# Performance work log

Measured on AMD Instinct MI355X. Metric: run time of the kernel, lower is better.

Reference implementation:

```python
import jax, jax.numpy as jnp
import numpy as np

B, F, D, M = 1024, 64, 256, 32
K = D // 3  # kWTA winners
LN_EPS = 1e-3  # keras LayerNormalization default


def setup_inputs() -> dict:
    key = jax.random.key(0)
    ks = jax.random.split(key, 8)
    in_dim = F * 2 * D  # flatten of concat([mean, var], -1)
    return {
        "mean_embeddings": jax.random.normal(ks[0], (B, F, D), jnp.float32),
        "var_embeddings": jax.random.uniform(ks[1], (B, F, D), jnp.float32),
        "W1": jax.random.normal(ks[2], (in_dim, D), jnp.float32) / np.sqrt(in_dim),
        "b1": jnp.zeros((D,), jnp.float32),
        "gamma": jnp.ones((D,), jnp.float32),
        "beta": jnp.zeros((D,), jnp.float32),
        "W2": jax.random.normal(ks[3], (D, M * D), jnp.float32) / np.sqrt(D),
        "b2": jnp.zeros((M * D,), jnp.float32),
    }


def _kwta(x, k):
    # exact top-k-by-|x| multi-hot mask, matching tf.one_hot + reduce_max
    idx = jax.lax.top_k(jnp.abs(x), k)[1]                      # (B, k)
    mask = jnp.zeros_like(x).at[jnp.arange(x.shape[0])[:, None], idx].set(1.0)
    return x * mask


def reference(mean_embeddings, var_embeddings, W1, b1, gamma, beta, W2, b2):
    x = jnp.concatenate([mean_embeddings, var_embeddings], axis=-1)  # (B, F, 2D)
    x = x.reshape(x.shape[0], -1)                                    # (B, F*2D)
    h = jax.nn.gelu(x @ W1 + b1, approximate=False)                  # (B, D)
    mu = jnp.mean(h, axis=-1, keepdims=True)
    var = jnp.mean(jnp.square(h - mu), axis=-1, keepdims=True)
    h = (h - mu) * jax.lax.rsqrt(var + LN_EPS) * gamma + beta        # LayerNorm
    h = _kwta(h, K)
    out = jnp.tanh(h @ W2 + b2)                                      # (B, M*D)
    return out.reshape(out.shape[0], M, D)
```

## Files before the change

### kernel.cpp

```cpp
#include <hip/hip_runtime.h>

typedef _Float16 f16;
typedef f16 f16x4 __attribute__((ext_vector_type(4)));
typedef f16 f16x8 __attribute__((ext_vector_type(8)));
typedef float f32x4 __attribute__((ext_vector_type(4)));

#define NB 1024
#define NF 64
#define ND 256
#define KWIN 85
#define INDIM 32768
#define OUTC 8192
#define MAXFIX 32
#define FKB 64
#define WSCALE 256.0f
#define LSCALE 2048.0f
#define INV_WS (1.0f / 256.0f)
#define INV_LS (1.0f / 2048.0f)

__device__ __forceinline__ int swz4(int row, int slot) { return slot ^ ((row ^ (row >> 2)) & 3); }
__device__ __forceinline__ int swz8(int row, int slot) { return slot ^ ((row ^ (row >> 3)) & 7); }

__device__ __forceinline__ void gl2lds16(const void* g, void* l) {
  __builtin_amdgcn_global_load_lds((const __attribute__((address_space(1))) void*)g,
                                   (__attribute__((address_space(3))) void*)l, 16, 0, 0);
}

__global__ __launch_bounds__(256) void transpose_split(const float* __restrict__ src,
                                                       f16* __restrict__ dhi, f16* __restrict__ dlo,
                                                       int R, int C) {
  __shared__ float tile[64][65];
  int t = threadIdx.x;
  int tiles_c = C >> 6;
  int tr = blockIdx.x / tiles_c, tc = blockIdx.x - tr * tiles_c;
  size_t r0 = (size_t)tr << 6;
  int c0 = tc << 6;
  int rr = t >> 4, cc = (t & 15) << 2;
#pragma unroll
  for (int p = 0; p < 4; ++p) {
    const float4 v = *(const float4*)(src + (r0 + (p << 4) + rr) * C + c0 + cc);
    tile[(p << 4) + rr][cc + 0] = v.x;
    tile[(p << 4) + rr][cc + 1] = v.y;
    tile[(p << 4) + rr][cc + 2] = v.z;
    tile[(p << 4) + rr][cc + 3] = v.w;
  }
  __syncthreads();
  int n = t >> 2, kq = t & 3;
  alignas(16) f16 hv[16];
  alignas(16) f16 lv[16];
#pragma unroll
  for (int e = 0; e < 16; ++e) {
    float x = tile[(kq << 4) + e][n] * WSCALE;
    f16 h = (f16)x;
    hv[e] = h;
    lv[e] = (f16)((x - (float)h) * LSCALE);
  }
  size_t ob = (size_t)(c0 + n) * (size_t)R + r0 + (kq << 4);
  *(f16x8*)(dhi + ob)     = *(const f16x8*)&hv[0];
  *(f16x8*)(dhi + ob + 8) = *(const f16x8*)&hv[8];
  *(f16x8*)(dlo + ob)     = *(const f16x8*)&lv[0];
  *(f16x8*)(dlo + ob + 8) = *(const f16x8*)&lv[8];
}

__global__ __launch_bounds__(512, 4) void gemm1_kernel(const float* __restrict__ meanp, const float* __restrict__ varp,
                                                       const f16* __restrict__ w1h, const f16* __restrict__ w1l,
                                                       float* __restrict__ partial) {
  __shared__ alignas(16) f16 sAh[128 * 32], sAl[128 * 32];
  __shared__ alignas(16) f16 sBh[128 * 32], sBl[128 * 32];
  int t = threadIdx.x;
  int chunk = blockIdx.x & 31;
  int nb = (blockIdx.x >> 5) & 1;
  int rb = blockIdx.x >> 6;
  int bm = rb << 7, bn = nb << 7;
  int wid = t >> 6, lane = t & 63, lr = lane & 15, lk = lane >> 4;
  int wr = wid >> 1, wc = wid & 1;
  f32x4 acc0[2][4] = {};
  f32x4 acc1[2][4] = {};
  int ar = t >> 3, ac4 = t & 7;
  int bnr = t >> 2, bslot = t & 3;

  for (int kk = 0; kk < 32; ++kk) {
    int gk = (chunk << 10) + (kk << 5);
    {
      size_t go = (size_t)(bn + bnr) * INDIM + (size_t)gk + (size_t)(swz4(bnr, bslot) << 3);
      gl2lds16(w1h + go, (char*)sBh + (wid << 10));
      gl2lds16(w1l + go, (char*)sBl + (wid << 10));
    }
    int f = gk >> 9, off = gk & 255;
    const float* xb = ((gk >> 8) & 1) ? varp : meanp;
#pragma unroll
    for (int p = 0; p < 2; ++p) {
      int row = ar + (p << 6);
      const float4 v = *(const float4*)(xb + ((size_t)(bm + row) * NF + f) * ND + off + (ac4 << 2));
      f16 h0 = (f16)v.x, h1 = (f16)v.y, h2 = (f16)v.z, h3 = (f16)v.w;
      f16x4 hv = {h0, h1, h2, h3};
      f16x4 lv = {(f16)((v.x - (float)h0) * LSCALE), (f16)((v.y - (float)h1) * LSCALE),
                  (f16)((v.z - (float)h2) * LSCALE), (f16)((v.w - (float)h3) * LSCALE)};
      int byte = (row << 6) + (swz4(row, ac4 >> 1) << 4) + ((ac4 & 1) << 3);
      *(f16x4*)((char*)sAh + byte) = hv;
      *(f16x4*)((char*)sAl + byte) = lv;
    }
    __syncthreads();
    f16x8 ah[2], al[2], bh[4], bl[4];
#pragma unroll
    for (int m = 0; m < 2; ++m) {
      int row = (wr << 5) + (m << 4) + lr;
      int byte = (row << 6) + (swz4(row, lk) << 4);
      ah[m] = *(const f16x8*)((const char*)sAh + byte);
      al[m] = *(const f16x8*)((const char*)sAl + byte);
    }
#pragma unroll
    for (int n = 0; n < 4; ++n) {
      int col = (wc << 6) + (n << 4) + lr;
      int byte = (col << 6) + (swz4(col, lk) << 4);
      bh[n] = *(const f16x8*)((const char*)sBh + byte);
      bl[n] = *(const f16x8*)((const char*)sBl + byte);
    }
#pragma unroll
    for (int m = 0; m < 2; ++m)
#pragma unroll
      for (int n = 0; n < 4; ++n) {
        acc0[m][n] = __builtin_amdgcn_mfma_f32_16x16x32_f16(ah[m], bh[n], acc0[m][n], 0, 0, 0);
        acc1[m][n] = __builtin_amdgcn_mfma_f32_16x16x32_f16(ah[m], bl[n], acc1[m][n], 0, 0, 0);
        acc1[m][n] = __builtin_amdgcn_mfma_f32_16x16x32_f16(al[m], bh[n], acc1[m][n], 0, 0, 0);
      }
    __syncthreads();
  }
  float* po = partial + (size_t)chunk * NB * ND;
#pragma unroll
  for (int m = 0; m < 2; ++m)
#pragma unroll
    for (int n = 0; n < 4; ++n)
#pragma unroll
      for (int r = 0; r < 4; ++r)
        po[(size_t)(bm + (wr << 5) + (m << 4) + (lk << 2) + r) * ND + bn + (wc << 6) + (n << 4) + lr] =
            (acc0[m][n][r] + acc1[m][n][r] * INV_LS) * INV_WS;
}

__device__ __forceinline__ double block_sum_f64(double v, double* sred) {
#pragma unroll
  for (int m = 32; m >= 1; m >>= 1) v += __shfl_xor(v, m);
  __syncthreads();
  if ((threadIdx.x & 63) == 0) sred[threadIdx.x >> 6] = v;
  __syncthreads();
  return sred[0] + sred[1] + sred[2] + sred[3];
}

__global__ __launch_bounds__(256) void reduce_ln_kwta(const float* __restrict__ partial, const float* __restrict__ b1,
                                                      const float* __restrict__ gamma, const float* __restrict__ beta,
                                                      f16* __restrict__ hh, f16* __restrict__ hl,
                                                      int* __restrict__ flags) {
  int b = blockIdx.x, d = threadIdx.x;
  double s = 0.0;
#pragma unroll
  for (int c = 0; c < 32; ++c) s += (double)partial[((size_t)c * NB + b) * ND + d];
  s += (double)b1[d];
  double g = 0.5 * s * (1.0 + erf(s * 0.70710678118654752440));
  __shared__ double sredd[4];
  double mu = block_sum_f64(g, sredd) * (1.0 / 256.0);
  double dv = g - mu;
  double var = block_sum_f64(dv * dv, sredd) * (1.0 / 256.0);
  double hn = dv * (1.0 / sqrt(var + 1e-3)) * (double)gamma[d] + (double)beta[d];
  double a = fabs(hn);
  __shared__ double as_[256];
  as_[d] = a;
  __syncthreads();
  int cnt_ex = 0;
  for (int j = 0; j < 256; ++j) {
    double aj = as_[j];
    cnt_ex += ((aj > a) || (aj == a && j < d)) ? 1 : 0;
  }
  __shared__ double a85, a86;
  if (cnt_ex == KWIN - 1) a85 = a;
  if (cnt_ex == KWIN) a86 = a;
  __syncthreads();
  const double M = 2e-5;
  if (d == 0 && (a85 - a86 < M)) {
    int slot = atomicAdd(&flags[0], 1);
    if (slot < MAXFIX) flags[1 + slot] = b;
  }
  float hv = (cnt_ex < KWIN) ? (float)hn : 0.f;
  f16 h = (f16)hv;
  size_t o = (size_t)b * ND + d;
  hh[o] = h;
  hl[o] = (f16)((hv - (float)h) * LSCALE);
}

__global__ __launch_bounds__(256) void fixup_gemv(const float* __restrict__ meanp, const float* __restrict__ varp,
                                                  const float* __restrict__ W1, const int* __restrict__ flags,
                                                  double* __restrict__ p64) {
  int nf = flags[0]; if (nf > MAXFIX) nf = MAXFIX;
  int slot = blockIdx.x >> 6;
  int kb = blockIdx.x & (FKB - 1);
  if (slot >= nf) return;
  int r = flags[1 + slot];
  int t = threadIdx.x;
  __shared__ float xs[512];
  int k0 = kb << 9;
  for (int i = t; i < 512; i += 256) {
    const float* xb = (i & 256) ? varp : meanp;
    xs[i] = xb[(((size_t)r * NF + kb) << 8) + (i & 255)];
  }
  __syncthreads();
  double accp0 = 0.0, accp1 = 0.0, acce0 = 0.0, acce1 = 0.0;
  const float* wcol = W1 + (size_t)k0 * ND + t;
#pragma unroll 8
  for (int i = 0; i < 512; i += 2) {
    float x0 = xs[i], w0 = wcol[(size_t)i * ND];
    float x1 = xs[i + 1], w1 = wcol[(size_t)(i + 1) * ND];
    float p0 = x0 * w0, p1 = x1 * w1;
    float e0 = fmaf(x0, w0, -p0), e1 = fmaf(x1, w1, -p1);
    accp0 += (double)p0;
    accp1 += (double)p1;
    acce0 += (double)e0;
    acce1 += (double)e1;
  }
  p64[((size_t)slot * FKB + kb) * ND + t] = (accp0 + accp1) + (acce0 + acce1);
}

__global__ __launch_bounds__(256) void fixup_ln_kwta(const double* __restrict__ p64, const float* __restrict__ b1,
                                                     const float* __restrict__ gamma, const float* __restrict__ beta,
                                                     const int* __restrict__ flags,
                                                     f16* __restrict__ hh, f16* __restrict__ hl) {
  int nf = flags[0]; if (nf > MAXFIX) nf = MAXFIX;
  int slot = blockIdx.x;
  if (slot >= nf) return;
  int r = flags[1 + slot];
  int d = threadIdx.x;
  double s = 0.0;
#pragma unroll
  for (int kb = 0; kb < FKB; ++kb) s += p64[((size_t)slot * FKB + kb) * ND + d];
  s += (double)b1[d];
  double g = 0.5 * s * (1.0 + erf(s * 0.70710678118654752440));
  __shared__ double sredd[4];
  double mu = block_sum_f64(g, sredd) * (1.0 / 256.0);
  double dv = g - mu;
  double var = block_sum_f64(dv * dv, sredd) * (1.0 / 256.0);
  double hn = dv * (1.0 / sqrt(var + 1e-3)) * (double)gamma[d] + (double)beta[d];
  double a = fabs(hn);
  __shared__ double as_[256];
  as_[d] = a;
  __syncthreads();
  int cnt = 0;
  for (int j = 0; j < 256; ++j) {
    double aj = as_[j];
    cnt += ((aj > a) || (aj == a && j < d)) ? 1 : 0;
  }
  double hvd = (cnt < KWIN) ? hn : 0.0;
  float hf = (float)hvd;
  f16 h = (f16)hf;
  size_t o = (size_t)r * ND + d;
  hh[o] = h;
  hl[o] = (f16)((hf - (float)h) * LSCALE);
}

__global__ __launch_bounds__(256, 2) void gemm2_kernel(const f16* __restrict__ hh, const f16* __restrict__ hl,
                                                       const f16* __restrict__ w2h, const f16* __restrict__ w2l,
                                                       const float* __restrict__ b2, float* __restrict__ outp) {
  __shared__ alignas(16) f16 sAh[128 * 64], sAl[128 * 64];
  __shared__ alignas(16) f16 sBh[128 * 64], sBl[128 * 64];
  int t = threadIdx.x;
  int bm = (blockIdx.x & 7) << 7;
  int bn = (blockIdx.x >> 3) << 7;
  int wid = t >> 6, lane = t & 63, lr = lane & 15, lk = lane >> 4;
  int wr = wid >> 1, wc = wid & 1;
  f32x4 acc0[4][4] = {};
  f32x4 acc1[4][4] = {};
  int amr = t >> 3, aslot = t & 7;

  for (int s = 0; s < 4; ++s) {
    int k0 = s << 6;
#pragma unroll
    for (int i = 0; i < 4; ++i) {
      int m = (i << 5) + amr;
      int ks = swz8(m, aslot) << 3;
      size_t goa = (size_t)(bm + m) * ND + k0 + ks;
      size_t gob = (size_t)(bn + m) * ND + k0 + ks;
      gl2lds16(hh + goa, (char*)sAh + (i << 12) + (wid << 10));
      gl2lds16(hl + goa, (char*)sAl + (i << 12) + (wid << 10));
      gl2lds16(w2h + gob, (char*)sBh + (i << 12) + (wid << 10));
      gl2lds16(w2l + gob, (char*)sBl + (i << 12) + (wid << 10));
    }
    __syncthreads();
#pragma unroll
    for (int k2 = 0; k2 < 2; ++k2) {
      int slot = (k2 << 2) + lk;
      f16x8 ah[4], al[4], bh[4], bl[4];
#pragma unroll
      for (int m = 0; m < 4; ++m) {
        int row = (wr << 6) + (m << 4) + lr;
        int byte = (row << 7) + (swz8(row, slot) << 4);
        ah[m] = *(const f16x8*)((const char*)sAh + byte);
        al[m] = *(const f16x8*)((const char*)sAl + byte);
      }
#pragma unroll
      for (int n = 0; n < 4; ++n) {
        int col = (wc << 6) + (n << 4) + lr;
        int byte = (col << 7) + (swz8(col, slot) << 4);
        bh[n] = *(const f16x8*)((const char*)sBh + byte);
        bl[n] = *(const f16x8*)((const char*)sBl + byte);
      }
#pragma unroll
      for (int m = 0; m < 4; ++m)
#pragma unroll
        for (int n = 0; n < 4; ++n) {
          acc0[m][n] = __builtin_amdgcn_mfma_f32_16x16x32_f16(ah[m], bh[n], acc0[m][n], 0, 0, 0);
          acc1[m][n] = __builtin_amdgcn_mfma_f32_16x16x32_f16(ah[m], bl[n], acc1[m][n], 0, 0, 0);
          acc1[m][n] = __builtin_amdgcn_mfma_f32_16x16x32_f16(al[m], bh[n], acc1[m][n], 0, 0, 0);
        }
    }
    __syncthreads();
  }
#pragma unroll
  for (int m = 0; m < 4; ++m)
#pragma unroll
    for (int n = 0; n < 4; ++n)
#pragma unroll
      for (int r = 0; r < 4; ++r) {
        int row = bm + (wr << 6) + (m << 4) + (lk << 2) + r;
        int col = bn + (wc << 6) + (n << 4) + lr;
        float val = (acc0[m][n][r] + acc1[m][n][r] * INV_LS) * INV_WS + b2[col];
        float av = fabsf(val);
        float e = __expf(-2.0f * av);
        float rr = (1.0f - e) / (1.0f + e);
        outp[(size_t)row * OUTC + col] = copysignf(rr, val);
      }
}

extern "C" void kernel_launch(void* const* d_in, const int* in_sizes, int n_in,
                              void* d_out, int out_size, void* d_ws, size_t ws_size,
                              hipStream_t stream) {
  (void)in_sizes; (void)n_in; (void)out_size; (void)ws_size;
  const float* meanp = (const float*)d_in[0];
  const float* varp  = (const float*)d_in[1];
  const float* W1    = (const float*)d_in[2];
  const float* b1    = (const float*)d_in[3];
  const float* gamma = (const float*)d_in[4];
  const float* beta  = (const float*)d_in[5];
  const float* W2    = (const float*)d_in[6];
  const float* b2    = (const float*)d_in[7];
  float* outp = (float*)d_out;
  char* ws = (char*)d_ws;

  f16* w1h = (f16*)(ws);
  f16* w1l = (f16*)(ws + ((size_t)16 << 20));
  f16* w2h = (f16*)(ws + ((size_t)32 << 20));
  f16* w2l = (f16*)(ws + ((size_t)36 << 20));
  float* partial = (float*)(ws + ((size_t)40 << 20));
  double* p64 = (double*)(ws + ((size_t)40 << 20));
  f16* hh = (f16*)(ws + ((size_t)72 << 20));
  f16* hl = (f16*)(ws + ((size_t)72 << 20) + ((size_t)512 << 10));
  int* flags = (int*)(ws + ((size_t)73 << 20));

  hipMemsetAsync(flags, 0, (1 + MAXFIX) * sizeof(int), stream);
  transpose_split<<<2048, 256, 0, stream>>>(W1, w1h, w1l, INDIM, ND);
  transpose_split<<<512, 256, 0, stream>>>(W2, w2h, w2l, ND, OUTC);
  gemm1_kernel<<<512, 512, 0, stream>>>(meanp, varp, w1h, w1l, partial);
  reduce_ln_kwta<<<NB, 256, 0, stream>>>(partial, b1, gamma, beta, hh, hl, flags);
  fixup_gemv<<<MAXFIX * FKB, 256, 0, stream>>>(meanp, varp, W1, flags, p64);
  fixup_ln_kwta<<<MAXFIX, 256, 0, stream>>>(p64, b1, gamma, beta, flags, hh, hl);
  gemm2_kernel<<<512, 256, 0, stream>>>(hh, hl, w2h, w2l, b2, outp);
}
```

Measured before the change: 186.9 us.

## Double-buffer LDS tiles in gemm1 and prefetch A into registers

Gemm1's shared-memory tiles become double-buffered. Each iteration now stages the next W1 tile via global_load_lds and writes the previous prefetched activation tile into the alternate buffer, then issues the global loads for two steps ahead before running MFMAs on the current buffer. This removes one barrier per iteration and lets global loads overlap with compute. In exchange, LDS use doubles to 64KB per block, which may lower occupancy under the 4-blocks launch bound. It also adds wrapped redundant loads at the tail (kk&31).

```diff
diff --git a/kernel.cpp b/kernel.cpp
--- a/kernel.cpp
+++ b/kernel.cpp
@@ -65,8 +65,8 @@
 __global__ __launch_bounds__(512, 4) void gemm1_kernel(const float* __restrict__ meanp, const float* __restrict__ varp,
                                                        const f16* __restrict__ w1h, const f16* __restrict__ w1l,
                                                        float* __restrict__ partial) {
-  __shared__ alignas(16) f16 sAh[128 * 32], sAl[128 * 32];
-  __shared__ alignas(16) f16 sBh[128 * 32], sBl[128 * 32];
+  __shared__ alignas(16) f16 sAh[2][128 * 32], sAl[2][128 * 32];
+  __shared__ alignas(16) f16 sBh[2][128 * 32], sBl[2][128 * 32];
   int t = threadIdx.x;
   int chunk = blockIdx.x & 31;
   int nb = (blockIdx.x >> 5) & 1;
@@ -79,42 +79,65 @@
   int ar = t >> 3, ac4 = t & 7;
   int bnr = t >> 2, bslot = t & 3;
 
-  for (int kk = 0; kk < 32; ++kk) {
-    int gk = (chunk << 10) + (kk << 5);
-    {
-      size_t go = (size_t)(bn + bnr) * INDIM + (size_t)gk + (size_t)(swz4(bnr, bslot) << 3);
-      gl2lds16(w1h + go, (char*)sBh + (wid << 10));
-      gl2lds16(w1l + go, (char*)sBl + (wid << 10));
-    }
-    int f = gk >> 9, off = gk & 255;
+  float4 fly[2];
+
+  auto STAGE_B = [&](int kkv, int buf) {
+    int gk = (chunk << 10) + ((kkv & 31) << 5);
+    size_t go = (size_t)(bn + bnr) * INDIM + (size_t)gk + (size_t)(swz4(bnr, bslot) << 3);
+    gl2lds16(w1h + go, (char*)&sBh[buf][0] + (wid << 10));
+    gl2lds16(w1l + go, (char*)&sBl[buf][0] + (wid << 10));
+  };
+  auto LOAD_A = [&](int kkv) {
+    int gk = (chunk << 10) + ((kkv & 31) << 5);
+    int f = gk >> 9, off = (gk & 255) + (ac4 << 2);
     const float* xb = ((gk >> 8) & 1) ? varp : meanp;
 #pragma unroll
     for (int p = 0; p < 2; ++p) {
       int row = ar + (p << 6);
-      const float4 v = *(const float4*)(xb + ((size_t)(bm + row) * NF + f) * ND + off + (ac4 << 2));
+      fly[p] = *(const float4*)(xb + ((size_t)(bm + row) * NF + f) * ND + off);
+    }
+  };
+  auto WRITE_A = [&](int buf) {
+#pragma unroll
+    for (int p = 0; p < 2; ++p) {
+      int row = ar + (p << 6);
+      float4 v = fly[p];
       f16 h0 = (f16)v.x, h1 = (f16)v.y, h2 = (f16)v.z, h3 = (f16)v.w;
       f16x4 hv = {h0, h1, h2, h3};
       f16x4 lv = {(f16)((v.x - (float)h0) * LSCALE), (f16)((v.y - (float)h1) * LSCALE),
                   (f16)((v.z - (float)h2) * LSCALE), (f16)((v.w - (float)h3) * LSCALE)};
       int byte = (row << 6) + (swz4(row, ac4 >> 1) << 4) + ((ac4 & 1) << 3);
-      *(f16x4*)((char*)sAh + byte) = hv;
-      *(f16x4*)((char*)sAl + byte) = lv;
-    }
-    __syncthreads();
+      *(f16x4*)((char*)&sAh[buf][0] + byte) = hv;
+      *(f16x4*)((char*)&sAl[buf][0] + byte) = lv;
+    }
+  };
+
+  STAGE_B(0, 0);
+  LOAD_A(0);
+  WRITE_A(0);
+  LOAD_A(1);
+  __syncthreads();
+
+  int cur = 0;
+  for (int kk = 0; kk < 32; ++kk) {
+    int nxt = cur ^ 1;
+    STAGE_B(kk + 1, nxt);
+    WRITE_A(nxt);
+    LOAD_A(kk + 2);
     f16x8 ah[2], al[2], bh[4], bl[4];
 #pragma unroll
     for (int m = 0; m < 2; ++m) {
       int row = (wr << 5) + (m << 4) + lr;
       int byte = (row << 6) + (swz4(row, lk) << 4);
-      ah[m] = *(const f16x8*)((const char*)sAh + byte);
-      al[m] = *(const f16x8*)((const char*)sAl + byte);
+      ah[m] = *(const f16x8*)((const char*)&sAh[cur][0] + byte);
+      al[m] = *(const f16x8*)((const char*)&sAl[cur][0] + byte);
     }
 #pragma unroll
     for (int n = 0; n < 4; ++n) {
       int col = (wc << 6) + (n << 4) + lr;
       int byte = (col << 6) + (swz4(col, lk) << 4);
-      bh[n] = *(const f16x8*)((const char*)sBh + byte);
-      bl[n] = *(const f16x8*)((const char*)sBl + byte);
+      bh[n] = *(const f16x8*)((const char*)&sBh[cur][0] + byte);
+      bl[n] = *(const f16x8*)((const char*)&sBl[cur][0] + byte);
     }
 #pragma unroll
     for (int m = 0; m < 2; ++m)
@@ -125,6 +148,7 @@
         acc1[m][n] = __builtin_amdgcn_mfma_f32_16x16x32_f16(al[m], bh[n], acc1[m][n], 0, 0, 0);
       }
     __syncthreads();
+    cur = nxt;
   }
   float* po = partial + (size_t)chunk * NB * ND;
 #pragma unroll
```

Result: no change. 185.4 us (-0.8%).
